# Performance work log

Hardware: AMD Instinct MI355X
Metric: run time of the kernel (lower is better)

The kernel has to match this reference:

```python
import jax, jax.numpy as jnp
import numpy as np

N_NODES = 170000
N_EDGES = 1200000
IN_DIM = 64
OUT_DIM = 40


def setup_inputs() -> dict:
    key = jax.random.key(0)
    k1, k2, k3, k4 = jax.random.split(key, 4)
    feats = jax.random.normal(k1, (N_NODES, IN_DIM), dtype=jnp.float32)
    # Linear layer params (Kaiming-ish scale)
    W = jax.random.normal(k2, (OUT_DIM, IN_DIM), dtype=jnp.float32) * (1.0 / np.sqrt(IN_DIM))
    b = jnp.zeros((OUT_DIM,), dtype=jnp.float32)
    src = jax.random.randint(k3, (N_EDGES,), 0, N_NODES, dtype=jnp.int64)
    dst = jax.random.randint(k4, (N_EDGES,), 0, N_NODES, dtype=jnp.int64)
    return {"feats": feats, "W": W, "b": b, "src": src, "dst": dst}


def reference(feats, W, b, src, dst):
    # DGL SGConv, k=1: symmetric normalization by in-degree^-1/2 on both sides.
    n = feats.shape[0]
    deg = jax.ops.segment_sum(jnp.ones_like(dst, dtype=feats.dtype), dst, num_segments=n)
    norm = jax.lax.rsqrt(jnp.maximum(deg, 1.0))  # clamp(min=1)
    h = feats * norm[:, None]                    # [N, D] pre-scale
    msgs = jnp.take(h, src, axis=0)              # [E, D] gather
    agg = jax.ops.segment_sum(msgs, dst, num_segments=n)  # [N, D] scatter-sum
    h = agg * norm[:, None]                      # post-scale
    out = jnp.einsum('nd,cd->nc', h, W) + b      # Linear(IN_DIM -> OUT_DIM)
    return out
```

## Files before the change

### kernel.cpp

```cpp
#include <hip/hip_runtime.h>
#include <hip/hip_bf16.h>

#define N_NODES 170000
#define N_EDGES 1200000
#define IN_DIM 64
#define OUT_DIM 40
#define PAD 32
#define ZW 20
#define MTILES (N_NODES / 16)
#define SEGS 8
#define SEG_SZ (N_NODES / SEGS)
#define SLICES 512
#define SLICE_E ((N_EDGES + SLICES - 1) / SLICES)

typedef __attribute__((ext_vector_type(8))) short short8;
typedef __attribute__((ext_vector_type(4))) float f32x4;

__device__ __forceinline__ float bf2f(unsigned int u) {
    union { unsigned int i; float f; } v;
    v.i = u << 16;
    return v.f;
}

__device__ __forceinline__ unsigned short f2bf_bits(float x) {
    __hip_bfloat16 h = __float2bfloat16(x);
    union { __hip_bfloat16 h; unsigned short u; } c; c.h = h;
    return c.u;
}

__device__ __forceinline__ int load_idx(const void* p, int e, int is_i32) {
    return is_i32 ? ((const int*)p)[e] : (int)((const long long*)p)[e];
}

__global__ void k_sniff_convert(const unsigned short* __restrict__ Wraw,
                                const unsigned short* __restrict__ braw,
                                const unsigned int* __restrict__ dstraw,
                                int* __restrict__ flags,
                                float* __restrict__ Wf, float* __restrict__ bf) {
    __shared__ int s_f32, s_i32;
    if (threadIdx.x == 0) { s_f32 = 0; s_i32 = 0; }
    __syncthreads();
    for (int i = threadIdx.x; i < OUT_DIM * IN_DIM; i += blockDim.x) {
        float v = bf2f(Wraw[i]);
        if (!(fabsf(v) <= 100.0f)) atomicOr(&s_f32, 1);
    }
    for (int i = threadIdx.x; i < 256; i += blockDim.x) {
        if (dstraw[2 * i + 1] != 0u) atomicOr(&s_i32, 1);
    }
    __syncthreads();
    int is_f32 = s_f32;
    if (threadIdx.x == 0) { flags[0] = s_f32; flags[1] = s_i32; }
    for (int i = threadIdx.x; i < OUT_DIM * IN_DIM; i += blockDim.x)
        Wf[i] = is_f32 ? ((const float*)Wraw)[i] : bf2f(Wraw[i]);
    for (int i = threadIdx.x; i < OUT_DIM; i += blockDim.x)
        bf[i] = is_f32 ? ((const float*)braw)[i] : bf2f(braw[i]);
}

__global__ void __launch_bounds__(256) k_fill(
    const void* __restrict__ src, const void* __restrict__ dst,
    int* __restrict__ cnt, int* __restrict__ slots,
    const int* __restrict__ flags) {
    int is_i32 = flags[1];
    int seg   = blockIdx.x & 7;
    int slice = blockIdx.x >> 3;
    int lo = seg * SEG_SZ, hi = lo + SEG_SZ;
    int e0 = slice * SLICE_E;
    int e1 = e0 + SLICE_E; if (e1 > N_EDGES) e1 = N_EDGES;
    for (int e = e0 + (int)threadIdx.x; e < e1; e += 256) {
        int d = load_idx(dst, e, is_i32);
        if (d >= lo && d < hi) {
            int s = load_idx(src, e, is_i32);
            int pos = atomicAdd(&cnt[d], 1);
            if (pos < PAD) slots[(size_t)d * PAD + pos] = s;
        }
    }
}

__global__ void __launch_bounds__(256) k_transform_mfma(
    const void* __restrict__ feats, const float* __restrict__ Wf,
    const int* __restrict__ cnt, unsigned short* __restrict__ Zp16,
    const int* __restrict__ flags) {
    int is_f32 = flags[0];
    int wave = (blockIdx.x * blockDim.x + threadIdx.x) >> 6;
    int lane = threadIdx.x & 63;
    if (wave >= MTILES) return;
    int m = lane & 15;
    int quad = lane >> 4;
    int node0 = wave * 16;

    short8 a0, a1;
    if (is_f32) {
        const float* frow = (const float*)feats + (size_t)(node0 + m) * IN_DIM + quad * 8;
        float4 p0 = *(const float4*)(frow + 0);
        float4 p1 = *(const float4*)(frow + 4);
        float4 p2 = *(const float4*)(frow + 32);
        float4 p3 = *(const float4*)(frow + 36);
        a0[0] = (short)f2bf_bits(p0.x); a0[1] = (short)f2bf_bits(p0.y);
        a0[2] = (short)f2bf_bits(p0.z); a0[3] = (short)f2bf_bits(p0.w);
        a0[4] = (short)f2bf_bits(p1.x); a0[5] = (short)f2bf_bits(p1.y);
        a0[6] = (short)f2bf_bits(p1.z); a0[7] = (short)f2bf_bits(p1.w);
        a1[0] = (short)f2bf_bits(p2.x); a1[1] = (short)f2bf_bits(p2.y);
        a1[2] = (short)f2bf_bits(p2.z); a1[3] = (short)f2bf_bits(p2.w);
        a1[4] = (short)f2bf_bits(p3.x); a1[5] = (short)f2bf_bits(p3.y);
        a1[6] = (short)f2bf_bits(p3.z); a1[7] = (short)f2bf_bits(p3.w);
    } else {
        const unsigned short* frow = (const unsigned short*)feats + (size_t)(node0 + m) * IN_DIM + quad * 8;
        ushort4 q0 = *(const ushort4*)(frow + 0);
        ushort4 q1 = *(const ushort4*)(frow + 4);
        ushort4 q2 = *(const ushort4*)(frow + 32);
        ushort4 q3 = *(const ushort4*)(frow + 36);
        a0[0] = (short)q0.x; a0[1] = (short)q0.y; a0[2] = (short)q0.z; a0[3] = (short)q0.w;
        a0[4] = (short)q1.x; a0[5] = (short)q1.y; a0[6] = (short)q1.z; a0[7] = (short)q1.w;
        a1[0] = (short)q2.x; a1[1] = (short)q2.y; a1[2] = (short)q2.z; a1[3] = (short)q2.w;
        a1[4] = (short)q3.x; a1[5] = (short)q3.y; a1[6] = (short)q3.z; a1[7] = (short)q3.w;
    }

    f32x4 c0 = {0.f, 0.f, 0.f, 0.f}, c1 = c0, c2 = c0;
#pragma unroll
    for (int t = 0; t < 3; t++) {
        int n = t * 16 + m;
        bool ok = (n < OUT_DIM);
        const float* wrow = Wf + (size_t)(ok ? n : 0) * IN_DIM + quad * 8;
        short8 b0, b1;
#pragma unroll
        for (int j = 0; j < 8; j++) { b0[j] = 0; b1[j] = 0; }
        if (ok) {
            float4 w0 = *(const float4*)(wrow + 0);
            float4 w1 = *(const float4*)(wrow + 4);
            float4 w2 = *(const float4*)(wrow + 32);
            float4 w3 = *(const float4*)(wrow + 36);
            b0[0] = (short)f2bf_bits(w0.x); b0[1] = (short)f2bf_bits(w0.y);
            b0[2] = (short)f2bf_bits(w0.z); b0[3] = (short)f2bf_bits(w0.w);
            b0[4] = (short)f2bf_bits(w1.x); b0[5] = (short)f2bf_bits(w1.y);
            b0[6] = (short)f2bf_bits(w1.z); b0[7] = (short)f2bf_bits(w1.w);
            b1[0] = (short)f2bf_bits(w2.x); b1[1] = (short)f2bf_bits(w2.y);
            b1[2] = (short)f2bf_bits(w2.z); b1[3] = (short)f2bf_bits(w2.w);
            b1[4] = (short)f2bf_bits(w3.x); b1[5] = (short)f2bf_bits(w3.y);
            b1[6] = (short)f2bf_bits(w3.z); b1[7] = (short)f2bf_bits(w3.w);
        }
        if (t == 0) {
            c0 = __builtin_amdgcn_mfma_f32_16x16x32_bf16(a0, b0, c0, 0, 0, 0);
            c0 = __builtin_amdgcn_mfma_f32_16x16x32_bf16(a1, b1, c0, 0, 0, 0);
        } else if (t == 1) {
            c1 = __builtin_amdgcn_mfma_f32_16x16x32_bf16(a0, b0, c1, 0, 0, 0);
            c1 = __builtin_amdgcn_mfma_f32_16x16x32_bf16(a1, b1, c1, 0, 0, 0);
        } else {
            c2 = __builtin_amdgcn_mfma_f32_16x16x32_bf16(a0, b0, c2, 0, 0, 0);
            c2 = __builtin_amdgcn_mfma_f32_16x16x32_bf16(a1, b1, c2, 0, 0, 0);
        }
    }

    int r0 = quad * 4;
    float nv[4];
#pragma unroll
    for (int r = 0; r < 4; r++) {
        int dg = cnt[node0 + r0 + r];
        nv[r] = rsqrtf(dg > 1 ? (float)dg : 1.0f);
    }
#pragma unroll
    for (int r = 0; r < 4; r++) {
        size_t base = (size_t)(node0 + r0 + r) * OUT_DIM;
        Zp16[base + m]      = f2bf_bits(c0[r] * nv[r]);
        Zp16[base + 16 + m] = f2bf_bits(c1[r] * nv[r]);
        if (m < 8)
            Zp16[base + 32 + m] = f2bf_bits(c2[r] * nv[r]);
    }
}

__global__ void __launch_bounds__(256) k_gather(
    const int* __restrict__ cnt, const int* __restrict__ slots,
    const unsigned int* __restrict__ Zp, const float* __restrict__ bf,
    float* __restrict__ out) {
    int wid = (blockIdx.x * blockDim.x + threadIdx.x) >> 6;
    int lane = threadIdx.x & 63;
    if (wid >= N_NODES) return;
    int deg = cnt[wid];
    int dc = deg > PAD ? PAD : deg;
    const int* sl = slots + (size_t)wid * PAD;
    int myslot = sl[lane & 31];

    int grp = lane / 10;
    int cidx = lane - grp * 10;
    bool lact = (grp < 6);

    float a0 = 0.f, a1 = 0.f, a2 = 0.f, a3 = 0.f;
    if (dc > 0) {
        int rounds = (dc + 5) / 6;
        bool v = lact && (grp < dc);
        int s = __shfl(myslot, (v ? grp : 0) & 31);
        uint2 r = *(const uint2*)(Zp + (size_t)s * ZW + 2 * cidx);
        for (int rd = 1; rd < rounds; rd++) {
            int e1 = rd * 6 + grp;
            bool v1 = lact && (e1 < dc);
            int s1 = __shfl(myslot, (v1 ? e1 : 0) & 31);
            uint2 rn = *(const uint2*)(Zp + (size_t)s1 * ZW + 2 * cidx);
            if (v) {
                a0 += bf2f(r.x & 0xFFFFu); a1 += bf2f(r.x >> 16);
                a2 += bf2f(r.y & 0xFFFFu); a3 += bf2f(r.y >> 16);
            }
            v = v1; r = rn;
        }
        if (v) {
            a0 += bf2f(r.x & 0xFFFFu); a1 += bf2f(r.x >> 16);
            a2 += bf2f(r.y & 0xFFFFu); a3 += bf2f(r.y >> 16);
        }
    }
    float b0 = a0 + __shfl(a0, (lane + 30) & 63);
    float b1 = a1 + __shfl(a1, (lane + 30) & 63);
    float b2 = a2 + __shfl(a2, (lane + 30) & 63);
    float b3 = a3 + __shfl(a3, (lane + 30) & 63);
    float t0 = b0 + __shfl(b0, (lane + 10) & 63) + __shfl(b0, (lane + 20) & 63);
    float t1 = b1 + __shfl(b1, (lane + 10) & 63) + __shfl(b1, (lane + 20) & 63);
    float t2 = b2 + __shfl(b2, (lane + 10) & 63) + __shfl(b2, (lane + 20) & 63);
    float t3 = b3 + __shfl(b3, (lane + 10) & 63) + __shfl(b3, (lane + 20) & 63);
    if (lane < 10) {
        float nv = rsqrtf(deg > 1 ? (float)deg : 1.0f);
        float4 o;
        o.x = fmaf(t0, nv, bf[4 * lane + 0]);
        o.y = fmaf(t1, nv, bf[4 * lane + 1]);
        o.z = fmaf(t2, nv, bf[4 * lane + 2]);
        o.w = fmaf(t3, nv, bf[4 * lane + 3]);
        *reinterpret_cast<float4*>(out + (size_t)wid * OUT_DIM + 4 * lane) = o;
    }
}

extern "C" void kernel_launch(void* const* d_in, const int* in_sizes, int n_in,
                              void* d_out, int out_size, void* d_ws, size_t ws_size,
                              hipStream_t stream) {
    const void* feats = d_in[0];
    const void* W     = d_in[1];
    const void* b     = d_in[2];
    const void* src   = d_in[3];
    const void* dst   = d_in[4];

    char* ws = (char*)d_ws;
    int*            flags = (int*)(ws + 0);
    float*          bf    = (float*)(ws + 256);
    float*          Wf    = (float*)(ws + 1024);
    int*            cnt   = (int*)(ws + 16384);
    int*            slots = (int*)(ws + 696448);
    unsigned short* Zp16  = (unsigned short*)(ws + 22456448);
    unsigned int*   Zp    = (unsigned int*)(ws + 22456448);

    (void)hipMemsetAsync(cnt, 0, 680000, stream);

    k_sniff_convert<<<1, 256, 0, stream>>>((const unsigned short*)W, (const unsigned short*)b,
                                           (const unsigned int*)dst, flags, Wf, bf);
    k_fill<<<SLICES * SEGS, 256, 0, stream>>>(src, dst, cnt, slots, flags);
    k_transform_mfma<<<(MTILES * 64 + 255) / 256, 256, 0, stream>>>(feats, Wf, cnt, Zp16, flags);
    k_gather<<<(N_NODES * 64 + 255) / 256, 256, 0, stream>>>(cnt, slots, Zp, bf, (float*)d_out);
}
```

Before: 224.0 us.

## Fuse edge fill with feature transform and move source-norm scaling into gather

The memset and sniff kernel are merged into one init kernel that zeroes the degree counts in parallel and pre-converts W to bf16. Edge bucketing and the MFMA feature transform now run as interleaved blocks of a single launch, so the transform no longer waits for degree counts. To make that legal, the source-side normalization is dropped from the transform and applied in the gather by reading cnt[src] per edge. This cuts launches and overlaps the atomic fill with the matmul, at the cost of an extra random cnt load and rsqrt per edge in the gather.

```diff
diff --git a/kernel.cpp b/kernel.cpp
--- a/kernel.cpp
+++ b/kernel.cpp
@@ -8,10 +8,13 @@
 #define PAD 32
 #define ZW 20
 #define MTILES (N_NODES / 16)
+#define TFB ((MTILES + 3) / 4)
 #define SEGS 8
 #define SEG_SZ (N_NODES / SEGS)
 #define SLICES 512
 #define SLICE_E ((N_EDGES + SLICES - 1) / SLICES)
+#define FILLB (SLICES * SEGS)
+#define FUSED_BLOCKS (FILLB + TFB)
 
 typedef __attribute__((ext_vector_type(8))) short short8;
 typedef __attribute__((ext_vector_type(4))) float f32x4;
@@ -32,144 +35,129 @@
     return is_i32 ? ((const int*)p)[e] : (int)((const long long*)p)[e];
 }
 
-__global__ void k_sniff_convert(const unsigned short* __restrict__ Wraw,
-                                const unsigned short* __restrict__ braw,
-                                const unsigned int* __restrict__ dstraw,
-                                int* __restrict__ flags,
-                                float* __restrict__ Wf, float* __restrict__ bf) {
+__global__ void __launch_bounds__(256) k_init(
+    const unsigned short* __restrict__ Wraw, const unsigned short* __restrict__ braw,
+    const unsigned int* __restrict__ dstraw, int* __restrict__ flags,
+    unsigned short* __restrict__ Wb, float* __restrict__ bfv, int* __restrict__ cnt) {
+    int tid = blockIdx.x * 256 + threadIdx.x;
+    int4* c4 = (int4*)cnt;
+    for (int i = tid; i < 42500; i += (int)gridDim.x * 256) c4[i] = make_int4(0, 0, 0, 0);
+    if (blockIdx.x != 0) return;
+
     __shared__ int s_f32, s_i32;
     if (threadIdx.x == 0) { s_f32 = 0; s_i32 = 0; }
     __syncthreads();
-    for (int i = threadIdx.x; i < OUT_DIM * IN_DIM; i += blockDim.x) {
+    for (int i = threadIdx.x; i < OUT_DIM * IN_DIM; i += 256) {
         float v = bf2f(Wraw[i]);
         if (!(fabsf(v) <= 100.0f)) atomicOr(&s_f32, 1);
     }
-    for (int i = threadIdx.x; i < 256; i += blockDim.x) {
+    for (int i = threadIdx.x; i < 256; i += 256) {
         if (dstraw[2 * i + 1] != 0u) atomicOr(&s_i32, 1);
     }
     __syncthreads();
     int is_f32 = s_f32;
     if (threadIdx.x == 0) { flags[0] = s_f32; flags[1] = s_i32; }
-    for (int i = threadIdx.x; i < OUT_DIM * IN_DIM; i += blockDim.x)
-        Wf[i] = is_f32 ? ((const float*)Wraw)[i] : bf2f(Wraw[i]);
-    for (int i = threadIdx.x; i < OUT_DIM; i += blockDim.x)
-        bf[i] = is_f32 ? ((const float*)braw)[i] : bf2f(braw[i]);
-}
-
-__global__ void __launch_bounds__(256) k_fill(
+    for (int i = threadIdx.x; i < OUT_DIM * IN_DIM; i += 256)
+        Wb[i] = is_f32 ? f2bf_bits(((const float*)Wraw)[i]) : Wraw[i];
+    for (int i = threadIdx.x; i < OUT_DIM; i += 256)
+        bfv[i] = is_f32 ? ((const float*)braw)[i] : bf2f(braw[i]);
+}
+
+__global__ void __launch_bounds__(256) k_fused(
     const void* __restrict__ src, const void* __restrict__ dst,
     int* __restrict__ cnt, int* __restrict__ slots,
-    const int* __restrict__ flags) {
-    int is_i32 = flags[1];
-    int seg   = blockIdx.x & 7;
-    int slice = blockIdx.x >> 3;
-    int lo = seg * SEG_SZ, hi = lo + SEG_SZ;
-    int e0 = slice * SLICE_E;
-    int e1 = e0 + SLICE_E; if (e1 > N_EDGES) e1 = N_EDGES;
-    for (int e = e0 + (int)threadIdx.x; e < e1; e += 256) {
-        int d = load_idx(dst, e, is_i32);
-        if (d >= lo && d < hi) {
-            int s = load_idx(src, e, is_i32);
-            int pos = atomicAdd(&cnt[d], 1);
-            if (pos < PAD) slots[(size_t)d * PAD + pos] = s;
-        }
-    }
-}
-
-__global__ void __launch_bounds__(256) k_transform_mfma(
-    const void* __restrict__ feats, const float* __restrict__ Wf,
-    const int* __restrict__ cnt, unsigned short* __restrict__ Zp16,
-    const int* __restrict__ flags) {
-    int is_f32 = flags[0];
-    int wave = (blockIdx.x * blockDim.x + threadIdx.x) >> 6;
-    int lane = threadIdx.x & 63;
-    if (wave >= MTILES) return;
-    int m = lane & 15;
-    int quad = lane >> 4;
-    int node0 = wave * 16;
-
-    short8 a0, a1;
-    if (is_f32) {
-        const float* frow = (const float*)feats + (size_t)(node0 + m) * IN_DIM + quad * 8;
-        float4 p0 = *(const float4*)(frow + 0);
-        float4 p1 = *(const float4*)(frow + 4);
-        float4 p2 = *(const float4*)(frow + 32);
-        float4 p3 = *(const float4*)(frow + 36);
-        a0[0] = (short)f2bf_bits(p0.x); a0[1] = (short)f2bf_bits(p0.y);
-        a0[2] = (short)f2bf_bits(p0.z); a0[3] = (short)f2bf_bits(p0.w);
-        a0[4] = (short)f2bf_bits(p1.x); a0[5] = (short)f2bf_bits(p1.y);
-        a0[6] = (short)f2bf_bits(p1.z); a0[7] = (short)f2bf_bits(p1.w);
-        a1[0] = (short)f2bf_bits(p2.x); a1[1] = (short)f2bf_bits(p2.y);
-        a1[2] = (short)f2bf_bits(p2.z); a1[3] = (short)f2bf_bits(p2.w);
-        a1[4] = (short)f2bf_bits(p3.x); a1[5] = (short)f2bf_bits(p3.y);
-        a1[6] = (short)f2bf_bits(p3.z); a1[7] = (short)f2bf_bits(p3.w);
+    const void* __restrict__ feats, const unsigned short* __restrict__ Wb,
+    unsigned short* __restrict__ Zp16, const int* __restrict__ flags) {
+    int bid = blockIdx.x;
+    int do_fill, id;
+    if (bid < 2 * TFB) { do_fill = bid & 1; id = bid >> 1; }
+    else               { do_fill = 1;       id = bid - TFB; }
+
+    if (do_fill) {
+        int is_i32 = flags[1];
+        int seg   = id & 7;
+        int slice = id >> 3;
+        int lo = seg * SEG_SZ, hi = lo + SEG_SZ;
+        int e0 = slice * SLICE_E;
+        int e1 = e0 + SLICE_E; if (e1 > N_EDGES) e1 = N_EDGES;
+        for (int e = e0 + (int)threadIdx.x; e < e1; e += 256) {
+            int d = load_idx(dst, e, is_i32);
+            if (d >= lo && d < hi) {
+                int s = load_idx(src, e, is_i32);
+                int pos = atomicAdd(&cnt[d], 1);
+                if (pos < PAD) slots[(size_t)d * PAD + pos] = s;
+            }
+        }
     } else {
-        const unsigned short* frow = (const unsigned short*)feats + (size_t)(node0 + m) * IN_DIM + quad * 8;
-        ushort4 q0 = *(const ushort4*)(frow + 0);
-        ushort4 q1 = *(const ushort4*)(frow + 4);
-        ushort4 q2 = *(const ushort4*)(frow + 32);
-        ushort4 q3 = *(const ushort4*)(frow + 36);
-        a0[0] = (short)q0.x; a0[1] = (short)q0.y; a0[2] = (short)q0.z; a0[3] = (short)q0.w;
-        a0[4] = (short)q1.x; a0[5] = (short)q1.y; a0[6] = (short)q1.z; a0[7] = (short)q1.w;
-        a1[0] = (short)q2.x; a1[1] = (short)q2.y; a1[2] = (short)q2.z; a1[3] = (short)q2.w;
-        a1[4] = (short)q3.x; a1[5] = (short)q3.y; a1[6] = (short)q3.z; a1[7] = (short)q3.w;
-    }
-
-    f32x4 c0 = {0.f, 0.f, 0.f, 0.f}, c1 = c0, c2 = c0;
+        int is_f32 = flags[0];
+        int wave = id * 4 + (int)(threadIdx.x >> 6);
+        int lane = threadIdx.x & 63;
+        if (wave >= MTILES) return;
+        int m = lane & 15;
+        int quad = lane >> 4;
+        int node0 = wave * 16;
+
+        short8 a0, a1;
+        if (is_f32) {
+            const float* frow = (const float*)feats + (size_t)(node0 + m) * IN_DIM + quad * 8;
+            float4 p0 = *(const float4*)(frow + 0);
+            float4 p1 = *(const float4*)(frow + 4);
+            float4 p2 = *(const float4*)(frow + 32);
+            float4 p3 = *(const float4*)(frow + 36);
+            a0[0] = (short)f2bf_bits(p0.x); a0[1] = (short)f2bf_bits(p0.y);
+            a0[2] = (short)f2bf_bits(p0.z); a0[3] = (short)f2bf_bits(p0.w);
+            a0[4] = (short)f2bf_bits(p1.x); a0[5] = (short)f2bf_bits(p1.y);
+            a0[6] = (short)f2bf_bits(p1.z); a0[7] = (short)f2bf_bits(p1.w);
+            a1[0] = (short)f2bf_bits(p2.x); a1[1] = (short)f2bf_bits(p2.y);
+            a1[2] = (short)f2bf_bits(p2.z); a1[3] = (short)f2bf_bits(p2.w);
+            a1[4] = (short)f2bf_bits(p3.x); a1[5] = (short)f2bf_bits(p3.y);
+            a1[6] = (short)f2bf_bits(p3.z); a1[7] = (short)f2bf_bits(p3.w);
+        } else {
+            const unsigned short* frow = (const unsigned short*)feats + (size_t)(node0 + m) * IN_DIM + quad * 8;
+            a0 = *(const short8*)(frow);
+            a1 = *(const short8*)(frow + 32);
+        }
+
+        f32x4 c0 = {0.f, 0.f, 0.f, 0.f}, c1 = c0, c2 = c0;
 #pragma unroll
-    for (int t = 0; t < 3; t++) {
-        int n = t * 16 + m;
-        bool ok = (n < OUT_DIM);
-        const float* wrow = Wf + (size_t)(ok ? n : 0) * IN_DIM + quad * 8;
-        short8 b0, b1;
+        for (int t = 0; t < 3; t++) {
+            int n = t * 16 + m;
+            bool ok = (n < OUT_DIM);
+            short8 b0, b1;
 #pragma unroll
-        for (int j = 0; j < 8; j++) { b0[j] = 0; b1[j] = 0; }
-        if (ok) {
-            float4 w0 = *(const float4*)(wrow + 0);
-            float4 w1 = *(const float4*)(wrow + 4);
-            float4 w2 = *(const float4*)(wrow + 32);
-            float4 w3 = *(const float4*)(wrow + 36);
-            b0[0] = (short)f2bf_bits(w0.x); b0[1] = (short)f2bf_bits(w0.y);
-            b0[2] = (short)f2bf_bits(w0.z); b0[3] = (short)f2bf_bits(w0.w);
-            b0[4] = (short)f2bf_bits(w1.x); b0[5] = (short)f2bf_bits(w1.y);
-            b0[6] = (short)f2bf_bits(w1.z); b0[7] = (short)f2bf_bits(w1.w);
-            b1[0] = (short)f2bf_bits(w2.x); b1[1] = (short)f2bf_bits(w2.y);
-            b1[2] = (short)f2bf_bits(w2.z); b1[3] = (short)f2bf_bits(w2.w);
-            b1[4] = (short)f2bf_bits(w3.x); b1[5] = (short)f2bf_bits(w3.y);
-            b1[6] = (short)f2bf_bits(w3.z); b1[7] = (short)f2bf_bits(w3.w);
-        }
-        if (t == 0) {
-            c0 = __builtin_amdgcn_mfma_f32_16x16x32_bf16(a0, b0, c0, 0, 0, 0);
-            c0 = __builtin_amdgcn_mfma_f32_16x16x32_bf16(a1, b1, c0, 0, 0, 0);
-        } else if (t == 1) {
-            c1 = __builtin_amdgcn_mfma_f32_16x16x32_bf16(a0, b0, c1, 0, 0, 0);
-            c1 = __builtin_amdgcn_mfma_f32_16x16x32_bf16(a1, b1, c1, 0, 0, 0);
-        } else {
-            c2 = __builtin_amdgcn_mfma_f32_16x16x32_bf16(a0, b0, c2, 0, 0, 0);
-            c2 = __builtin_amdgcn_mfma_f32_16x16x32_bf16(a1, b1, c2, 0, 0, 0);
-        }
-    }
-
-    int r0 = quad * 4;
-    float nv[4];
+            for (int j = 0; j < 8; j++) { b0[j] = 0; b1[j] = 0; }
+            if (ok) {
+                const unsigned short* wrow = Wb + (size_t)n * IN_DIM + quad * 8;
+                b0 = *(const short8*)(wrow);
+                b1 = *(const short8*)(wrow + 32);
+            }
+            if (t == 0) {
+                c0 = __builtin_amdgcn_mfma_f32_16x16x32_bf16(a0, b0, c0, 0, 0, 0);
+                c0 = __builtin_amdgcn_mfma_f32_16x16x32_bf16(a1, b1, c0, 0, 0, 0);
+            } else if (t == 1) {
+                c1 = __builtin_amdgcn_mfma_f32_16x16x32_bf16(a0, b0, c1, 0, 0, 0);
+                c1 = __builtin_amdgcn_mfma_f32_16x16x32_bf16(a1, b1, c1, 0, 0, 0);
+            } else {
+                c2 = __builtin_amdgcn_mfma_f32_16x16x32_bf16(a0, b0, c2, 0, 0, 0);
+                c2 = __builtin_amdgcn_mfma_f32_16x16x32_bf16(a1, b1, c2, 0, 0, 0);
+            }
+        }
+
+        int r0 = quad * 4;
 #pragma unroll
-    for (int r = 0; r < 4; r++) {
-        int dg = cnt[node0 + r0 + r];
-        nv[r] = rsqrtf(dg > 1 ? (float)dg : 1.0f);
-    }
-#pragma unroll
-    for (int r = 0; r < 4; r++) {
-        size_t base = (size_t)(node0 + r0 + r) * OUT_DIM;
-        Zp16[base + m]      = f2bf_bits(c0[r] * nv[r]);
-        Zp16[base + 16 + m] = f2bf_bits(c1[r] * nv[r]);
-        if (m < 8)
-            Zp16[base + 32 + m] = f2bf_bits(c2[r] * nv[r]);
+        for (int r = 0; r < 4; r++) {
+            size_t base = (size_t)(node0 + r0 + r) * OUT_DIM;
+            Zp16[base + m]      = f2bf_bits(c0[r]);
+            Zp16[base + 16 + m] = f2bf_bits(c1[r]);
+            if (m < 8)
+                Zp16[base + 32 + m] = f2bf_bits(c2[r]);
+        }
     }
 }
 
 __global__ void __launch_bounds__(256) k_gather(
     const int* __restrict__ cnt, const int* __restrict__ slots,
-    const unsigned int* __restrict__ Zp, const float* __restrict__ bf,
+    const unsigned int* __restrict__ Zp, const float* __restrict__ bfv,
     float* __restrict__ out) {
     int wid = (blockIdx.x * blockDim.x + threadIdx.x) >> 6;
     int lane = threadIdx.x & 63;
@@ -189,20 +177,28 @@
         bool v = lact && (grp < dc);
         int s = __shfl(myslot, (v ? grp : 0) & 31);
         uint2 r = *(const uint2*)(Zp + (size_t)s * ZW + 2 * cidx);
+        int cdeg = cnt[s];
         for (int rd = 1; rd < rounds; rd++) {
             int e1 = rd * 6 + grp;
             bool v1 = lact && (e1 < dc);
             int s1 = __shfl(myslot, (v1 ? e1 : 0) & 31);
             uint2 rn = *(const uint2*)(Zp + (size_t)s1 * ZW + 2 * cidx);
+            int cn = cnt[s1];
             if (v) {
-                a0 += bf2f(r.x & 0xFFFFu); a1 += bf2f(r.x >> 16);
-                a2 += bf2f(r.y & 0xFFFFu); a3 += bf2f(r.y >> 16);
-            }
-            v = v1; r = rn;
+                float nvs = rsqrtf(cdeg > 1 ? (float)cdeg : 1.0f);
+                a0 = fmaf(bf2f(r.x & 0xFFFFu), nvs, a0);
+                a1 = fmaf(bf2f(r.x >> 16),     nvs, a1);
+                a2 = fmaf(bf2f(r.y & 0xFFFFu), nvs, a2);
+                a3 = fmaf(bf2f(r.y >> 16),     nvs, a3);
+            }
+            v = v1; r = rn; cdeg = cn;
         }
         if (v) {
-            a0 += bf2f(r.x & 0xFFFFu); a1 += bf2f(r.x >> 16);
-            a2 += bf2f(r.y & 0xFFFFu); a3 += bf2f(r.y >> 16);
+            float nvs = rsqrtf(cdeg > 1 ? (float)cdeg : 1.0f);
+            a0 = fmaf(bf2f(r.x & 0xFFFFu), nvs, a0);
+            a1 = fmaf(bf2f(r.x >> 16),     nvs, a1);
+            a2 = fmaf(bf2f(r.y & 0xFFFFu), nvs, a2);
+            a3 = fmaf(bf2f(r.y >> 16),     nvs, a3);
         }
     }
     float b0 = a0 + __shfl(a0, (lane + 30) & 63);
@@ -216,10 +212,10 @@
     if (lane < 10) {
         float nv = rsqrtf(deg > 1 ? (float)deg : 1.0f);
         float4 o;
-        o.x = fmaf(t0, nv, bf[4 * lane + 0]);
-        o.y = fmaf(t1, nv, bf[4 * lane + 1]);
-        o.z = fmaf(t2, nv, bf[4 * lane + 2]);
-        o.w = fmaf(t3, nv, bf[4 * lane + 3]);
+        o.x = fmaf(t0, nv, bfv[4 * lane + 0]);
+        o.y = fmaf(t1, nv, bfv[4 * lane + 1]);
+        o.z = fmaf(t2, nv, bfv[4 * lane + 2]);
+        o.w = fmaf(t3, nv, bfv[4 * lane + 3]);
         *reinterpret_cast<float4*>(out + (size_t)wid * OUT_DIM + 4 * lane) = o;
     }
 }
@@ -235,18 +231,15 @@
 
     char* ws = (char*)d_ws;
     int*            flags = (int*)(ws + 0);
-    float*          bf    = (float*)(ws + 256);
-    float*          Wf    = (float*)(ws + 1024);
+    float*          bfv   = (float*)(ws + 256);
+    unsigned short* Wb    = (unsigned short*)(ws + 1024);
     int*            cnt   = (int*)(ws + 16384);
     int*            slots = (int*)(ws + 696448);
     unsigned short* Zp16  = (unsigned short*)(ws + 22456448);
     unsigned int*   Zp    = (unsigned int*)(ws + 22456448);
 
-    (void)hipMemsetAsync(cnt, 0, 680000, stream);
-
-    k_sniff_convert<<<1, 256, 0, stream>>>((const unsigned short*)W, (const unsigned short*)b,
-                                           (const unsigned int*)dst, flags, Wf, bf);
-    k_fill<<<SLICES * SEGS, 256, 0, stream>>>(src, dst, cnt, slots, flags);
-    k_transform_mfma<<<(MTILES * 64 + 255) / 256, 256, 0, stream>>>(feats, Wf, cnt, Zp16, flags);
-    k_gather<<<(N_NODES * 64 + 255) / 256, 256, 0, stream>>>(cnt, slots, Zp, bf, (float*)d_out);
-}
+    k_init<<<256, 256, 0, stream>>>((const unsigned short*)W, (const unsigned short*)b,
+                                    (const unsigned int*)dst, flags, Wb, bfv, cnt);
+    k_fused<<<FUSED_BLOCKS, 256, 0, stream>>>(src, dst, cnt, slots, feats, Wb, Zp16, flags);
+    k_gather<<<(N_NODES * 64 + 255) / 256, 256, 0, stream>>>(cnt, slots, Zp, bfv, (float*)d_out);
+}
```

After: 199.2 us. 11.1% less time.
